# Optimization experiments

Measured on AMD Instinct MI355X. Metric: run time of the kernel, lower is better.

## Reference

```python
import jax, jax.numpy as jnp
import numpy as np

N = 100000      # nodes
E = 1600000     # edges (before self-loops)
FIN = 128       # in_channels
HID = 16        # hidden_channels
H = 8           # heads (layer 1)
OUT = 64        # out_channels
LN_EPS = 1e-5


def setup_inputs() -> dict:
    key = jax.random.key(0)
    ks = jax.random.split(key, 24)
    def p(i, shape):
        return jax.random.normal(ks[i], shape, dtype=jnp.float32) * 0.05
    return {
        "x": jax.random.normal(ks[0], (N, FIN), dtype=jnp.float32),
        "edge_index": jax.random.randint(ks[1], (2, E), 0, N, dtype=jnp.int32),
        # GATv2 layer 1: in -> H*HID, concat
        "Wl1": p(2, (FIN, H * HID)), "bl1": p(3, (H * HID,)),
        "Wr1": p(4, (FIN, H * HID)), "br1": p(5, (H * HID,)),
        "att1": p(6, (H, HID)), "bias1": p(7, (H * HID,)),
        # GATv2 layer 2: H*HID -> HID, heads=1
        "Wl2": p(8, (H * HID, HID)), "bl2": p(9, (HID,)),
        "Wr2": p(10, (H * HID, HID)), "br2": p(11, (HID,)),
        "att2": p(12, (1, HID)), "bias2": p(13, (HID,)),
        # LayerNorms
        "ln1_g": jnp.ones((H * HID,), jnp.float32), "ln1_b": jnp.zeros((H * HID,), jnp.float32),
        "ln2_g": jnp.ones((HID,), jnp.float32), "ln2_b": jnp.zeros((HID,), jnp.float32),
        # residual / skip / output linears
        "res1_W": p(14, (FIN, H * HID)), "res1_b": p(15, (H * HID,)),
        "res2_W": p(16, (H * HID, HID)), "res2_b": p(17, (HID,)),
        "skip_W": p(18, (H * HID, HID)), "skip_b": p(19, (HID,)),
        "out_W": p(20, (HID, OUT)), "out_b": p(21, (OUT,)),
    }


def _layernorm(x, g, b):
    mu = jnp.mean(x, axis=-1, keepdims=True)
    var = jnp.mean((x - mu) ** 2, axis=-1, keepdims=True)
    return (x - mu) * jax.lax.rsqrt(var + LN_EPS) * g + b


def _gatv2(x, src, dst, Wl, bl, Wr, br, att, bias, concat):
    # PyG GATv2Conv (share_weights=False, eval mode): message from src j to dst i
    Hh, C = att.shape
    n = x.shape[0]
    xl = (x @ Wl + bl).reshape(n, Hh, C)   # source-side transform
    xr = (x @ Wr + br).reshape(n, Hh, C)   # target-side transform
    m = xl[src] + xr[dst]                  # [E, H, C]
    e = jax.nn.leaky_relu(m, 0.2)
    alpha = jnp.einsum('ehc,hc->eh', e, att)          # [E, H]
    amax = jax.ops.segment_max(alpha, dst, num_segments=n)
    alpha = jnp.exp(alpha - amax[dst])
    denom = jax.ops.segment_sum(alpha, dst, num_segments=n)
    alpha = alpha / (denom[dst] + 1e-16)
    out = jax.ops.segment_sum(xl[src] * alpha[:, :, None], dst, num_segments=n)  # [N, H, C]
    out = out.reshape(n, Hh * C) if concat else out.mean(axis=1)
    return out + bias


def reference(x, edge_index, Wl1, bl1, Wr1, br1, att1, bias1,
              Wl2, bl2, Wr2, br2, att2, bias2,
              ln1_g, ln1_b, ln2_g, ln2_b,
              res1_W, res1_b, res2_W, res2_b, skip_W, skip_b, out_W, out_b):
    n = x.shape[0]
    loops = jnp.arange(n, dtype=edge_index.dtype)
    src = jnp.concatenate([edge_index[0], loops])
    dst = jnp.concatenate([edge_index[1], loops])

    h = _gatv2(x, src, dst, Wl1, bl1, Wr1, br1, att1, bias1, concat=True)
    h = _layernorm(h, ln1_g, ln1_b)
    h = h + (x @ res1_W + res1_b)
    h = jax.nn.elu(h)            # dropout off in eval

    skip_in = h
    h2 = _gatv2(h, src, dst, Wl2, bl2, Wr2, br2, att2, bias2, concat=False)
    h2 = _layernorm(h2, ln2_g, ln2_b)
    h2 = h2 + (skip_in @ res2_W + res2_b)
    h2 = jax.nn.elu(h2)
    h2 = h2 + (skip_in @ skip_W + skip_b)
    return h2 @ out_W + out_b
```

## Files before the change

### kernel.cpp

```cpp
#include <hip/hip_runtime.h>

typedef __attribute__((ext_vector_type(8))) short bf16x8;
typedef __attribute__((ext_vector_type(4))) float f32x4;

__device__ __forceinline__ float bf2f(ushort u) {
  union { uint i; float f; } v; v.i = ((uint)u) << 16; return v.f;
}
__device__ __forceinline__ ushort f2bf(float f) {
  union { float f; uint i; } v; v.f = f;
  uint r = (v.i + 0x7FFFu + ((v.i >> 16) & 1u)) >> 16;
  return (ushort)r;
}

template <int CTRL>
__device__ __forceinline__ float dppadd(float x) {
  union { float f; int i; } a, b;
  a.f = x;
  b.i = __builtin_amdgcn_update_dpp(0, a.i, CTRL, 0xF, 0xF, true);
  return a.f + b.f;
}
#define DPP_X1 0xB1
#define DPP_X2 0x4E
#define DPP_X7 0x141
#define DPP_XF 0x140


__global__ __launch_bounds__(256) void k_zero(int* p, int n) {
  int i = blockIdx.x * 256 + threadIdx.x;
  if (i < n) p[i] = 0;
}

__global__ __launch_bounds__(256) void k_hist(const int* __restrict__ ei, int* __restrict__ cnt, int E) {
  int e = blockIdx.x * 256 + threadIdx.x;
  if (e < E) atomicAdd(&cnt[ei[E + e]], 1);
}

__global__ __launch_bounds__(256) void k_scan1(const int* __restrict__ cnt, int* __restrict__ partial, int n) {
  int i = blockIdx.x * 256 + threadIdx.x;
  int v = (i < n) ? cnt[i] : 0;
  #pragma unroll
  for (int m = 1; m < 64; m <<= 1) v += __shfl_xor(v, m);
  __shared__ int sm[4];
  if ((threadIdx.x & 63) == 0) sm[threadIdx.x >> 6] = v;
  __syncthreads();
  if (threadIdx.x == 0) partial[blockIdx.x] = sm[0] + sm[1] + sm[2] + sm[3];
}

__global__ __launch_bounds__(512) void k_scan2(int* partial, int nb) {
  __shared__ int buf[2][512];
  int t = threadIdx.x;
  int v = (t < nb) ? partial[t] : 0;
  buf[0][t] = v;
  __syncthreads();
  int cur = 0;
  for (int off = 1; off < 512; off <<= 1) {
    int x = buf[cur][t];
    if (t >= off) x += buf[cur][t - off];
    buf[cur ^ 1][t] = x;
    __syncthreads();
    cur ^= 1;
  }
  if (t < nb) partial[t] = buf[cur][t] - v;
}

__global__ __launch_bounds__(256) void k_scan3(const int* __restrict__ cnt, const int* __restrict__ partial,
                                               int* __restrict__ rowptr, int* __restrict__ cursor, int n) {
  __shared__ int buf[2][256];
  int t = threadIdx.x;
  int i = blockIdx.x * 256 + t;
  int v = (i < n) ? cnt[i] : 0;
  buf[0][t] = v;
  __syncthreads();
  int cur = 0;
  for (int off = 1; off < 256; off <<= 1) {
    int x = buf[cur][t];
    if (t >= off) x += buf[cur][t - off];
    buf[cur ^ 1][t] = x;
    __syncthreads();
    cur ^= 1;
  }
  if (i < n) {
    int incl = buf[cur][t];
    int base = partial[blockIdx.x];
    int rp = base + incl - v;
    rowptr[i] = rp;
    cursor[i] = rp;
    if (i == n - 1) rowptr[n] = base + incl;
  }
}

__global__ __launch_bounds__(256) void k_scatter(const int* __restrict__ ei, int* __restrict__ cursor,
                                                 int* __restrict__ ssrc, int E, int NS) {
  int t = threadIdx.x;
  int base = blockIdx.x * 2048;
  int src[8], dst[8];
  #pragma unroll
  for (int j = 0; j < 8; ++j) {
    int idx = base + j * 256 + t;
    bool ok = idx < E;
    src[j] = ok ? ei[idx] : 0;
    dst[j] = ok ? ei[E + idx] : -1;
  }
  for (int s = 0; s < NS; ++s) {
    #pragma unroll
    for (int j = 0; j < 8; ++j) {
      if ((dst[j] >> 13) == s) {
        int pos = atomicAdd(&cursor[dst[j]], 1);
        ssrc[pos] = src[j];
      }
    }
  }
}


__global__ __launch_bounds__(256) void k_conv(const float* __restrict__ x, ushort* __restrict__ AF, int total) {
  int t = blockIdx.x * 256 + threadIdx.x;
  if (t >= total) return;
  int m = t >> 4, k8 = t & 15;
  const float* src = x + (size_t)m * 128 + k8 * 8;
  float4 f0 = *(const float4*)src;
  float4 f1 = *(const float4*)(src + 4);
  uint4 o;
  o.x = f2bf(f0.x) | ((uint)f2bf(f0.y) << 16);
  o.y = f2bf(f0.z) | ((uint)f2bf(f0.w) << 16);
  o.z = f2bf(f1.x) | ((uint)f2bf(f1.y) << 16);
  o.w = f2bf(f1.z) | ((uint)f2bf(f1.w) << 16);
  size_t off = ((size_t)(((m >> 4) * 4 + (k8 >> 2)) * 64) + (m & 15) + ((k8 & 3) << 4)) * 8;
  *(uint4*)(AF + off) = o;
}


__global__ __launch_bounds__(256) void k_pack(
    const float* __restrict__ Wl1, const float* __restrict__ bl1,
    const float* __restrict__ Wr1, const float* __restrict__ br1,
    const float* __restrict__ res1W, const float* __restrict__ res1b,
    const float* __restrict__ Wl2, const float* __restrict__ bl2,
    const float* __restrict__ Wr2, const float* __restrict__ br2,
    const float* __restrict__ res2W, const float* __restrict__ res2b,
    const float* __restrict__ skipW, const float* __restrict__ skipb,
    const float* __restrict__ att1, const float* __restrict__ att2,
    ushort* __restrict__ W1F, float* __restrict__ B1P,
    ushort* __restrict__ W2F, float* __restrict__ B2P,
    float* __restrict__ attE, float* __restrict__ at2E) {
  const float LOG2E = 1.4426950408889634f;
  int tid = blockIdx.x * 256 + threadIdx.x;
  if (tid < 49152) {
    int j = tid & 7, l = (tid >> 3) & 63, ktile = (tid >> 9) & 3, ct = tid >> 11;
    int k = ktile * 32 + ((l >> 4) << 3) + j;
    int n = ct * 16 + (l & 15);
    int sel = n >> 7, jj = n & 127;
    const float* s = sel == 0 ? Wl1 : sel == 1 ? Wr1 : res1W;
    W1F[tid] = f2bf(s[k * 128 + jj]);
  } else if (tid < 57344) {
    int u = tid - 49152;
    int j = u & 7, l = (u >> 3) & 63, ktile = (u >> 9) & 3, ct = u >> 11;
    int k = ktile * 32 + ((l >> 4) << 3) + j;
    int n = ct * 16 + (l & 15);
    int sel = n >> 4, jj = n & 15;
    const float* s = sel == 0 ? Wl2 : sel == 1 ? Wr2 : sel == 2 ? res2W : skipW;
    W2F[u] = f2bf(s[k * 16 + jj]);
  } else if (tid < 57728) {
    int n = tid - 57344;
    int sel = n >> 7, jj = n & 127;
    const float* sb = sel == 0 ? bl1 : sel == 1 ? br1 : res1b;
    B1P[n] = sb[jj];
  } else if (tid < 57792) {
    int n = tid - 57728;
    int sel = n >> 4, jj = n & 15;
    const float* sb = sel == 0 ? bl2 : sel == 1 ? br2 : sel == 2 ? res2b : skipb;
    B2P[n] = sb[jj];
  } else if (tid < 57920) {
    int n = tid - 57792;
    attE[n] = att1[n] * LOG2E;
  } else if (tid < 57936) {
    int n = tid - 57920;
    at2E[n] = att2[n] * LOG2E;
  }
}


__global__ __launch_bounds__(256) void k_mfma(
    const ushort* __restrict__ AF, const ushort* __restrict__ WF,
    const float* __restrict__ bias,
    ushort* __restrict__ O0, ushort* __restrict__ O1,
    ushort* __restrict__ O2, ushort* __restrict__ O3,
    int M, int cs_shift) {
  int w = threadIdx.x >> 6, l = threadIdx.x & 63;
  int m0 = blockIdx.x * 64;
  int c0 = blockIdx.y * 64 + w * 16;
  int ct = c0 >> 4;
  f32x4 acc[4] = {};
  #pragma unroll
  for (int kt = 0; kt < 4; ++kt) {
    bf16x8 b = *(const bf16x8*)(WF + ((size_t)((ct * 4 + kt) * 64 + l)) * 8);
    #pragma unroll
    for (int rt = 0; rt < 4; ++rt) {
      bf16x8 a = *(const bf16x8*)(AF + ((size_t)((blockIdx.x * 16 + rt * 4 + kt) * 64 + l)) * 8);
      acc[rt] = __builtin_amdgcn_mfma_f32_16x16x32_bf16(a, b, acc[rt], 0, 0, 0);
    }
  }
  int col = c0 + (l & 15);
  int arr = col >> cs_shift;
  ushort* O = arr == 0 ? O0 : arr == 1 ? O1 : arr == 2 ? O2 : O3;
  int stride = 1 << cs_shift;
  int lcol = col & (stride - 1);
  float bv = bias[col];
  int rbase = m0 + ((l >> 4) << 2);
  #pragma unroll
  for (int rt = 0; rt < 4; ++rt) {
    #pragma unroll
    for (int r = 0; r < 4; ++r) {
      int m = rbase + rt * 16 + r;
      if (m < M) O[(size_t)m * stride + lcol] = f2bf(acc[rt][r] + bv);
    }
  }
}


#define EDGE1U(u)                                                          \
  {                                                                        \
    float vx = __builtin_bit_cast(float, (u) << 16);                       \
    float vy = __builtin_bit_cast(float, (u) & 0xffff0000u);               \
    float mx = vx + xr.x, my = vy + xr.y;                                  \
    float ta = atv.x * mx + atv.y * my;                                    \
    float tb = atv.x * __builtin_fabsf(mx) + atv.y * __builtin_fabsf(my);  \
    float tt = 0.6f * ta + 0.4f * tb;                                      \
    tt = dppadd<DPP_X1>(tt);                                               \
    tt = dppadd<DPP_X2>(tt);                                               \
    tt = dppadd<DPP_X7>(tt);                                               \
    float p = __builtin_amdgcn_exp2f(tt);                                  \
    accx += p * vx; accy += p * vy; den += p;                              \
  }

__global__ __launch_bounds__(256) void k_gat1(
    const ushort* __restrict__ XLG, const ushort* __restrict__ XR,
    const ushort* __restrict__ RE,
    const float* __restrict__ attE, const float* __restrict__ bias1,
    const float* __restrict__ g1, const float* __restrict__ b1,
    const int* __restrict__ rowptr, const int* __restrict__ ssrc,
    ushort* __restrict__ HF, int n) {
  int lane = threadIdx.x & 63;
  int i = blockIdx.x * 4 + (threadIdx.x >> 6);
  if (i >= n) return;
  int f = lane * 2;
  size_t ib = (size_t)i << 7;
  uint u_self = *(const uint*)(XLG + ib + f);
  float2 xr;
  { uint u = *(const uint*)(XR + ib + f);
    xr = make_float2(__builtin_bit_cast(float, u << 16),
                     __builtin_bit_cast(float, u & 0xffff0000u)); }
  float2 atv = *(const float2*)&attE[f];
  float accx = 0.f, accy = 0.f, den = 0.f;
  EDGE1U(u_self);
  int e0 = __builtin_amdgcn_readfirstlane(rowptr[i]);
  int e1 = __builtin_amdgcn_readfirstlane(rowptr[i + 1]);
  for (int base = e0; base < e1; base += 64) {
    int cnt = e1 - base; if (cnt > 64) cnt = 64;
    int sidx = ssrc[base + (lane < cnt ? lane : cnt - 1)];
    int j = 0;
    for (; j + 4 <= cnt; j += 4) {
      int s0 = __builtin_amdgcn_readlane(sidx, j);
      int s1 = __builtin_amdgcn_readlane(sidx, j + 1);
      int s2 = __builtin_amdgcn_readlane(sidx, j + 2);
      int s3 = __builtin_amdgcn_readlane(sidx, j + 3);
      uint u0 = *(const uint*)(XLG + ((size_t)(uint)s0 << 7) + f);
      uint u1 = *(const uint*)(XLG + ((size_t)(uint)s1 << 7) + f);
      uint u2 = *(const uint*)(XLG + ((size_t)(uint)s2 << 7) + f);
      uint u3 = *(const uint*)(XLG + ((size_t)(uint)s3 << 7) + f);
      EDGE1U(u0); EDGE1U(u1); EDGE1U(u2); EDGE1U(u3);
    }
    for (; j < cnt; ++j) {
      int s = __builtin_amdgcn_readlane(sidx, j);
      uint u = *(const uint*)(XLG + ((size_t)(uint)s << 7) + f);
      EDGE1U(u);
    }
  }
  float inv = 1.f / (den + 1e-16f);
  float2 bv = *(const float2*)&bias1[f];
  float ox = accx * inv + bv.x, oy = accy * inv + bv.y;
  float s = ox + oy;
  #pragma unroll
  for (int m = 1; m < 64; m <<= 1) s += __shfl_xor(s, m);
  float mu = s * (1.f / 128.f);
  float dx = ox - mu, dy = oy - mu;
  float q = dx * dx + dy * dy;
  #pragma unroll
  for (int m = 1; m < 64; m <<= 1) q += __shfl_xor(q, m);
  float rstd = rsqrtf(q * (1.f / 128.f) + 1e-5f);
  float2 gg = *(const float2*)&g1[f];
  float2 bb = *(const float2*)&b1[f];
  float2 rv;
  { uint u = *(const uint*)(RE + ib + f);
    rv = make_float2(__builtin_bit_cast(float, u << 16),
                     __builtin_bit_cast(float, u & 0xffff0000u)); }
  float yx = dx * rstd * gg.x + bb.x + rv.x;
  float yy = dy * rstd * gg.y + bb.y + rv.y;
  yx = yx > 0.f ? yx : __expf(yx) - 1.f;
  yy = yy > 0.f ? yy : __expf(yy) - 1.f;
  size_t off = (((size_t)(i >> 4) * 4 + (lane >> 4)) * 64 + (i & 15) + ((lane >> 2) & 3) * 16) * 8
               + 2 * (lane & 3);
  *(uint*)(HF + off) = (uint)f2bf(yx) | ((uint)f2bf(yy) << 16);
}


#define EDGE2V(v)                                            \
  {                                                          \
    float m = (v) + xr;                                      \
    float ta = a2 * m;                                       \
    float tb = a2 * __builtin_fabsf(m);                      \
    float tt = 0.6f * ta + 0.4f * tb;                        \
    tt = dppadd<DPP_X1>(tt);                                 \
    tt = dppadd<DPP_X2>(tt);                                 \
    tt = dppadd<DPP_X7>(tt);                                 \
    tt = dppadd<DPP_XF>(tt);                                 \
    float p = __builtin_amdgcn_exp2f(tt);                    \
    acc += p * (v); den += p;                                \
  }

__global__ __launch_bounds__(256) void k_gat2(
    const ushort* __restrict__ XG, const ushort* __restrict__ XRr,
    const ushort* __restrict__ XE, const ushort* __restrict__ XS,
    const float* __restrict__ at2E, const float* __restrict__ bias2,
    const float* __restrict__ g2, const float* __restrict__ b2,
    const int* __restrict__ rowptr, const int* __restrict__ ssrc,
    const float* __restrict__ outW, const float* __restrict__ outB,
    float* __restrict__ Out, int n) {
  __shared__ float sW[1024];
  __shared__ float sB[64];
  int t = threadIdx.x;
  for (int idx = t; idx < 1024; idx += 256) sW[idx] = outW[idx];
  if (t < 64) sB[t] = outB[t];
  __syncthreads();
  int c = t & 15;
  int i = blockIdx.x * 16 + (t >> 4);
  if (i >= n) return;
  size_t ib = (size_t)i << 4;
  float xl = bf2f(XG[ib + c]), xr = bf2f(XRr[ib + c]);
  float resv = bf2f(XE[ib + c]), skipv = bf2f(XS[ib + c]);
  float a2 = at2E[c];
  float acc = 0.f, den = 0.f;
  EDGE2V(xl);
  int e0 = rowptr[i], e1 = rowptr[i + 1];
  int e = e0;
  for (; e + 4 <= e1; e += 4) {
    int s0 = ssrc[e], s1 = ssrc[e + 1], s2 = ssrc[e + 2], s3 = ssrc[e + 3];
    float v0 = bf2f(XG[((size_t)(uint)s0 << 4) + c]);
    float v1 = bf2f(XG[((size_t)(uint)s1 << 4) + c]);
    float v2 = bf2f(XG[((size_t)(uint)s2 << 4) + c]);
    float v3 = bf2f(XG[((size_t)(uint)s3 << 4) + c]);
    EDGE2V(v0); EDGE2V(v1); EDGE2V(v2); EDGE2V(v3);
  }
  for (; e < e1; ++e) {
    int s = ssrc[e];
    float v = bf2f(XG[((size_t)(uint)s << 4) + c]);
    EDGE2V(v);
  }
  float o = acc / (den + 1e-16f) + bias2[c];
  float s = o;
  s = dppadd<DPP_X1>(s); s = dppadd<DPP_X2>(s); s = dppadd<DPP_X7>(s); s = dppadd<DPP_XF>(s);
  float mu = s * (1.f / 16.f);
  float d = o - mu;
  float q = d * d;
  q = dppadd<DPP_X1>(q); q = dppadd<DPP_X2>(q); q = dppadd<DPP_X7>(q); q = dppadd<DPP_XF>(q);
  float rstd = rsqrtf(q * (1.f / 16.f) + 1e-5f);
  float y = d * rstd * g2[c] + b2[c] + resv;
  y = y > 0.f ? y : __expf(y) - 1.f;
  y += skipv;
  float a0 = sB[c * 4 + 0], a1 = sB[c * 4 + 1], ao2 = sB[c * 4 + 2], a3 = sB[c * 4 + 3];
  #pragma unroll
  for (int cc = 0; cc < 16; ++cc) {
    float h = __shfl(y, cc, 16);
    a0 += h * sW[cc * 64 + c * 4 + 0];
    a1 += h * sW[cc * 64 + c * 4 + 1];
    ao2 += h * sW[cc * 64 + c * 4 + 2];
    a3 += h * sW[cc * 64 + c * 4 + 3];
  }
  *(float4*)&Out[(size_t)i * 64 + c * 4] = make_float4(a0, a1, ao2, a3);
}


extern "C" void kernel_launch(void* const* d_in, const int* in_sizes, int n_in,
                              void* d_out, int out_size, void* d_ws, size_t ws_size,
                              hipStream_t stream) {
  const float* x     = (const float*)d_in[0];
  const int*   ei    = (const int*)d_in[1];
  const float* Wl1   = (const float*)d_in[2];
  const float* bl1   = (const float*)d_in[3];
  const float* Wr1   = (const float*)d_in[4];
  const float* br1   = (const float*)d_in[5];
  const float* att1  = (const float*)d_in[6];
  const float* bias1 = (const float*)d_in[7];
  const float* Wl2   = (const float*)d_in[8];
  const float* bl2   = (const float*)d_in[9];
  const float* Wr2   = (const float*)d_in[10];
  const float* br2   = (const float*)d_in[11];
  const float* att2  = (const float*)d_in[12];
  const float* bias2 = (const float*)d_in[13];
  const float* ln1g  = (const float*)d_in[14];
  const float* ln1b  = (const float*)d_in[15];
  const float* ln2g  = (const float*)d_in[16];
  const float* ln2b  = (const float*)d_in[17];
  const float* res1W = (const float*)d_in[18];
  const float* res1b = (const float*)d_in[19];
  const float* res2W = (const float*)d_in[20];
  const float* res2b = (const float*)d_in[21];
  const float* skipW = (const float*)d_in[22];
  const float* skipb = (const float*)d_in[23];
  const float* outW  = (const float*)d_in[24];
  const float* outb  = (const float*)d_in[25];
  int N = in_sizes[0] / 128;
  int E = in_sizes[1] / 2;
  float* out = (float*)d_out;

  int nblk = (N + 63) / 64;
  int ngrp = nblk * 4;

  ushort* XF   = (ushort*)d_ws;
  ushort* XLG  = XF + (size_t)ngrp * 2048;
  ushort* XR1  = XLG + (size_t)N * 128;
  ushort* RE1  = XR1 + (size_t)N * 128;
  ushort* HF   = RE1 + (size_t)N * 128;
  ushort* XG2  = HF + (size_t)ngrp * 2048;
  ushort* X2R  = XG2 + (size_t)N * 16;
  ushort* X2E  = X2R + (size_t)N * 16;
  ushort* X2S  = X2E + (size_t)N * 16;
  ushort* W1F  = X2S + (size_t)N * 16;
  ushort* W2F  = W1F + 49152;
  float*  B1P  = (float*)(W2F + 8192);
  float*  B2P  = B1P + 384;
  float*  attE = B2P + 64;
  float*  at2E = attE + 128;
  int* cnt     = (int*)(at2E + 16);
  int* cursor  = cnt + N;
  int* rowptr  = cursor + N;
  int* ssrc    = rowptr + N + 1;
  int* partial = ssrc + E;

  int nbS = (N + 255) / 256;
  int nbE = (E + 255) / 256;
  int NS = ((N - 1) >> 13) + 1;

  k_pack<<<227, 256, 0, stream>>>(Wl1, bl1, Wr1, br1, res1W, res1b,
                                  Wl2, bl2, Wr2, br2, res2W, res2b, skipW, skipb,
                                  att1, att2, W1F, B1P, W2F, B2P, attE, at2E);
  k_conv<<<(N * 16 + 255) / 256, 256, 0, stream>>>(x, XF, N * 16);

  k_zero<<<nbS, 256, 0, stream>>>(cnt, N);
  k_hist<<<nbE, 256, 0, stream>>>(ei, cnt, E);
  k_scan1<<<nbS, 256, 0, stream>>>(cnt, partial, N);
  k_scan2<<<1, 512, 0, stream>>>(partial, nbS);
  k_scan3<<<nbS, 256, 0, stream>>>(cnt, partial, rowptr, cursor, N);
  k_scatter<<<(E + 2047) / 2048, 256, 0, stream>>>(ei, cursor, ssrc, E, NS);

  dim3 g1g(nblk, 6);
  k_mfma<<<g1g, 256, 0, stream>>>(XF, W1F, B1P, XLG, XR1, RE1, XLG, N, 7);

  k_gat1<<<(N + 3) / 4, 256, 0, stream>>>(XLG, XR1, RE1, attE, bias1, ln1g, ln1b,
                                          rowptr, ssrc, HF, N);

  dim3 g2g(nblk, 1);
  k_mfma<<<g2g, 256, 0, stream>>>(HF, W2F, B2P, XG2, X2R, X2E, X2S, N, 4);
  k_gat2<<<(N + 15) / 16, 256, 0, stream>>>(XG2, X2R, X2E, X2S, at2E, bias2, ln2g, ln2b,
                                            rowptr, ssrc, outW, outb, out, N);
}
```

Measured before the change: 487.6 us.

## Fuse setup kernels, merge scatter with GEMM, and widen gat1 edge loads

Merges weight packing, x conversion and count zeroing into one init kernel. The scan2 pass is dropped because each scan3 block now sums its preceding partials itself. CSR scatter and the layer-1 MFMA GEMM run as independent blocks of one launch, and the histogram processes four edges per thread. The gat1 kernel is restructured so each half-wave handles a different edge with 4 features per lane, using pre-split 0.6/0.4 attention weights to simplify the leaky-relu dot product. Together these aim to cut launch count and the per-edge reduction cost, at the price of more complex indexing and redundant partial summation in the scan.

```diff
diff --git a/kernel.cpp b/kernel.cpp
--- a/kernel.cpp
+++ b/kernel.cpp
@@ -11,6 +11,8 @@
   uint r = (v.i + 0x7FFFu + ((v.i >> 16) & 1u)) >> 16;
   return (ushort)r;
 }
+__device__ __forceinline__ float blo(uint u) { return __builtin_bit_cast(float, u << 16); }
+__device__ __forceinline__ float bhi(uint u) { return __builtin_bit_cast(float, u & 0xffff0000u); }
 
 template <int CTRL>
 __device__ __forceinline__ float dppadd(float x) {
@@ -25,15 +27,93 @@
 #define DPP_XF 0x140
 
 
-__global__ __launch_bounds__(256) void k_zero(int* p, int n) {
-  int i = blockIdx.x * 256 + threadIdx.x;
-  if (i < n) p[i] = 0;
-}
+__global__ __launch_bounds__(256) void k_init(
+    const float* __restrict__ x, ushort* __restrict__ XF,
+    const float* __restrict__ Wl1, const float* __restrict__ bl1,
+    const float* __restrict__ Wr1, const float* __restrict__ br1,
+    const float* __restrict__ res1W, const float* __restrict__ res1b,
+    const float* __restrict__ Wl2, const float* __restrict__ bl2,
+    const float* __restrict__ Wr2, const float* __restrict__ br2,
+    const float* __restrict__ res2W, const float* __restrict__ res2b,
+    const float* __restrict__ skipW, const float* __restrict__ skipb,
+    const float* __restrict__ att1, const float* __restrict__ att2,
+    ushort* __restrict__ W1F, float* __restrict__ B1P,
+    ushort* __restrict__ W2F, float* __restrict__ B2P,
+    float* __restrict__ at6, float* __restrict__ at4, float* __restrict__ at2E,
+    int* __restrict__ cnt, int N) {
+  const float LOG2E = 1.4426950408889634f;
+  int b = blockIdx.x, t = threadIdx.x;
+  int CB = (N * 16 + 255) >> 8;
+  if (b < 227) {
+    int tid = b * 256 + t;
+    if (tid < 49152) {
+      int j = tid & 7, l = (tid >> 3) & 63, ktile = (tid >> 9) & 3, ct = tid >> 11;
+      int k = ktile * 32 + ((l >> 4) << 3) + j;
+      int n = ct * 16 + (l & 15);
+      int sel = n >> 7, jj = n & 127;
+      const float* s = sel == 0 ? Wl1 : sel == 1 ? Wr1 : res1W;
+      W1F[tid] = f2bf(s[k * 128 + jj]);
+    } else if (tid < 57344) {
+      int u = tid - 49152;
+      int j = u & 7, l = (u >> 3) & 63, ktile = (u >> 9) & 3, ct = u >> 11;
+      int k = ktile * 32 + ((l >> 4) << 3) + j;
+      int n = ct * 16 + (l & 15);
+      int sel = n >> 4, jj = n & 15;
+      const float* s = sel == 0 ? Wl2 : sel == 1 ? Wr2 : sel == 2 ? res2W : skipW;
+      W2F[u] = f2bf(s[k * 16 + jj]);
+    } else if (tid < 57728) {
+      int n = tid - 57344;
+      int sel = n >> 7, jj = n & 127;
+      const float* sb = sel == 0 ? bl1 : sel == 1 ? br1 : res1b;
+      B1P[n] = sb[jj];
+    } else if (tid < 57792) {
+      int n = tid - 57728;
+      int sel = n >> 4, jj = n & 15;
+      const float* sb = sel == 0 ? bl2 : sel == 1 ? br2 : sel == 2 ? res2b : skipb;
+      B2P[n] = sb[jj];
+    } else if (tid < 57920) {
+      int n = tid - 57792;
+      at6[n] = att1[n] * 0.6f * LOG2E;
+    } else if (tid < 58048) {
+      int n = tid - 57920;
+      at4[n] = att1[n] * 0.4f * LOG2E;
+    } else if (tid < 58064) {
+      int n = tid - 58048;
+      at2E[n] = att2[n] * LOG2E;
+    }
+  } else if (b < 227 + CB) {
+    int t2 = (b - 227) * 256 + t;
+    if (t2 < N * 16) {
+      int m = t2 >> 4, k8 = t2 & 15;
+      const float* src = x + (size_t)m * 128 + k8 * 8;
+      float4 f0 = *(const float4*)src;
+      float4 f1 = *(const float4*)(src + 4);
+      uint4 o;
+      o.x = f2bf(f0.x) | ((uint)f2bf(f0.y) << 16);
+      o.y = f2bf(f0.z) | ((uint)f2bf(f0.w) << 16);
+      o.z = f2bf(f1.x) | ((uint)f2bf(f1.y) << 16);
+      o.w = f2bf(f1.z) | ((uint)f2bf(f1.w) << 16);
+      size_t off = ((size_t)(((m >> 4) * 4 + (k8 >> 2)) * 64) + (m & 15) + ((k8 & 3) << 4)) * 8;
+      *(uint4*)(XF + off) = o;
+    }
+  } else {
+    int idx = (b - 227 - CB) * 256 + t;
+    if (idx < N) cnt[idx] = 0;
+  }
+}
+
 
 __global__ __launch_bounds__(256) void k_hist(const int* __restrict__ ei, int* __restrict__ cnt, int E) {
-  int e = blockIdx.x * 256 + threadIdx.x;
-  if (e < E) atomicAdd(&cnt[ei[E + e]], 1);
-}
+  int e4 = (blockIdx.x * 256 + threadIdx.x) * 4;
+  if (e4 + 3 < E) {
+    int4 d = *(const int4*)&ei[E + e4];
+    atomicAdd(&cnt[d.x], 1); atomicAdd(&cnt[d.y], 1);
+    atomicAdd(&cnt[d.z], 1); atomicAdd(&cnt[d.w], 1);
+  } else {
+    for (int e = e4; e < E; ++e) atomicAdd(&cnt[ei[E + e]], 1);
+  }
+}
+
 
 __global__ __launch_bounds__(256) void k_scan1(const int* __restrict__ cnt, int* __restrict__ partial, int n) {
   int i = blockIdx.x * 256 + threadIdx.x;
@@ -46,28 +126,21 @@
   if (threadIdx.x == 0) partial[blockIdx.x] = sm[0] + sm[1] + sm[2] + sm[3];
 }
 
-__global__ __launch_bounds__(512) void k_scan2(int* partial, int nb) {
-  __shared__ int buf[2][512];
+
+__global__ __launch_bounds__(256) void k_scan3lb(const int* __restrict__ cnt, const int* __restrict__ partial,
+                                                 int* __restrict__ rowptr, int* __restrict__ cursor, int n) {
   int t = threadIdx.x;
-  int v = (t < nb) ? partial[t] : 0;
-  buf[0][t] = v;
+  int b = blockIdx.x;
+  int acc = 0;
+  for (int j = t; j < b; j += 256) acc += partial[j];
+  #pragma unroll
+  for (int m = 1; m < 64; m <<= 1) acc += __shfl_xor(acc, m);
+  __shared__ int sm[4];
+  if ((t & 63) == 0) sm[t >> 6] = acc;
   __syncthreads();
-  int cur = 0;
-  for (int off = 1; off < 512; off <<= 1) {
-    int x = buf[cur][t];
-    if (t >= off) x += buf[cur][t - off];
-    buf[cur ^ 1][t] = x;
-    __syncthreads();
-    cur ^= 1;
-  }
-  if (t < nb) partial[t] = buf[cur][t] - v;
-}
-
-__global__ __launch_bounds__(256) void k_scan3(const int* __restrict__ cnt, const int* __restrict__ partial,
-                                               int* __restrict__ rowptr, int* __restrict__ cursor, int n) {
+  int base = sm[0] + sm[1] + sm[2] + sm[3];
   __shared__ int buf[2][256];
-  int t = threadIdx.x;
-  int i = blockIdx.x * 256 + t;
+  int i = b * 256 + t;
   int v = (i < n) ? cnt[i] : 0;
   buf[0][t] = v;
   __syncthreads();
@@ -81,7 +154,6 @@
   }
   if (i < n) {
     int incl = buf[cur][t];
-    int base = partial[blockIdx.x];
     int rp = base + incl - v;
     rowptr[i] = rp;
     cursor[i] = rp;
@@ -89,105 +161,77 @@
   }
 }
 
-__global__ __launch_bounds__(256) void k_scatter(const int* __restrict__ ei, int* __restrict__ cursor,
-                                                 int* __restrict__ ssrc, int E, int NS) {
+
+__global__ __launch_bounds__(256) void k_scatgemm(
+    const int* __restrict__ ei, int* __restrict__ cursor, int* __restrict__ ssrc, int E, int NS, int nScat,
+    const ushort* __restrict__ AF, const ushort* __restrict__ WF, const float* __restrict__ bias,
+    ushort* __restrict__ O0, ushort* __restrict__ O1, ushort* __restrict__ O2,
+    int M, int nblk) {
+  int b = blockIdx.x;
   int t = threadIdx.x;
-  int base = blockIdx.x * 2048;
-  int src[8], dst[8];
-  #pragma unroll
-  for (int j = 0; j < 8; ++j) {
-    int idx = base + j * 256 + t;
-    bool ok = idx < E;
-    src[j] = ok ? ei[idx] : 0;
-    dst[j] = ok ? ei[E + idx] : -1;
-  }
-  for (int s = 0; s < NS; ++s) {
+  if (b < nScat) {
+    int base = b * 2048;
+    int src[8], dst[8];
     #pragma unroll
     for (int j = 0; j < 8; ++j) {
-      if ((dst[j] >> 13) == s) {
-        int pos = atomicAdd(&cursor[dst[j]], 1);
-        ssrc[pos] = src[j];
+      int idx = base + j * 256 + t;
+      bool ok = idx < E;
+      src[j] = ok ? ei[idx] : 0;
+      dst[j] = ok ? ei[E + idx] : -1;
+    }
+    for (int s = 0; s < NS; ++s) {
+      #pragma unroll
+      for (int j = 0; j < 8; ++j) {
+        if ((dst[j] >> 13) == s) {
+          int pos = atomicAdd(&cursor[dst[j]], 1);
+          ssrc[pos] = src[j];
+        }
       }
     }
-  }
-}
-
-
-__global__ __launch_bounds__(256) void k_conv(const float* __restrict__ x, ushort* __restrict__ AF, int total) {
-  int t = blockIdx.x * 256 + threadIdx.x;
-  if (t >= total) return;
-  int m = t >> 4, k8 = t & 15;
-  const float* src = x + (size_t)m * 128 + k8 * 8;
-  float4 f0 = *(const float4*)src;
-  float4 f1 = *(const float4*)(src + 4);
-  uint4 o;
-  o.x = f2bf(f0.x) | ((uint)f2bf(f0.y) << 16);
-  o.y = f2bf(f0.z) | ((uint)f2bf(f0.w) << 16);
-  o.z = f2bf(f1.x) | ((uint)f2bf(f1.y) << 16);
-  o.w = f2bf(f1.z) | ((uint)f2bf(f1.w) << 16);
-  size_t off = ((size_t)(((m >> 4) * 4 + (k8 >> 2)) * 64) + (m & 15) + ((k8 & 3) << 4)) * 8;
-  *(uint4*)(AF + off) = o;
-}
-
-
-__global__ __launch_bounds__(256) void k_pack(
-    const float* __restrict__ Wl1, const float* __restrict__ bl1,
-    const float* __restrict__ Wr1, const float* __restrict__ br1,
-    const float* __restrict__ res1W, const float* __restrict__ res1b,
-    const float* __restrict__ Wl2, const float* __restrict__ bl2,
-    const float* __restrict__ Wr2, const float* __restrict__ br2,
-    const float* __restrict__ res2W, const float* __restrict__ res2b,
-    const float* __restrict__ skipW, const float* __restrict__ skipb,
-    const float* __restrict__ att1, const float* __restrict__ att2,
-    ushort* __restrict__ W1F, float* __restrict__ B1P,
-    ushort* __restrict__ W2F, float* __restrict__ B2P,
-    float* __restrict__ attE, float* __restrict__ at2E) {
-  const float LOG2E = 1.4426950408889634f;
-  int tid = blockIdx.x * 256 + threadIdx.x;
-  if (tid < 49152) {
-    int j = tid & 7, l = (tid >> 3) & 63, ktile = (tid >> 9) & 3, ct = tid >> 11;
-    int k = ktile * 32 + ((l >> 4) << 3) + j;
-    int n = ct * 16 + (l & 15);
-    int sel = n >> 7, jj = n & 127;
-    const float* s = sel == 0 ? Wl1 : sel == 1 ? Wr1 : res1W;
-    W1F[tid] = f2bf(s[k * 128 + jj]);
-  } else if (tid < 57344) {
-    int u = tid - 49152;
-    int j = u & 7, l = (u >> 3) & 63, ktile = (u >> 9) & 3, ct = u >> 11;
-    int k = ktile * 32 + ((l >> 4) << 3) + j;
-    int n = ct * 16 + (l & 15);
-    int sel = n >> 4, jj = n & 15;
-    const float* s = sel == 0 ? Wl2 : sel == 1 ? Wr2 : sel == 2 ? res2W : skipW;
-    W2F[u] = f2bf(s[k * 16 + jj]);
-  } else if (tid < 57728) {
-    int n = tid - 57344;
-    int sel = n >> 7, jj = n & 127;
-    const float* sb = sel == 0 ? bl1 : sel == 1 ? br1 : res1b;
-    B1P[n] = sb[jj];
-  } else if (tid < 57792) {
-    int n = tid - 57728;
-    int sel = n >> 4, jj = n & 15;
-    const float* sb = sel == 0 ? bl2 : sel == 1 ? br2 : sel == 2 ? res2b : skipb;
-    B2P[n] = sb[jj];
-  } else if (tid < 57920) {
-    int n = tid - 57792;
-    attE[n] = att1[n] * LOG2E;
-  } else if (tid < 57936) {
-    int n = tid - 57920;
-    at2E[n] = att2[n] * LOG2E;
-  }
-}
-
-
-__global__ __launch_bounds__(256) void k_mfma(
+  } else {
+    int bb = b - nScat;
+    int by = bb / nblk;
+    int bx = bb - by * nblk;
+    int w = t >> 6, l = t & 63;
+    int m0 = bx * 64;
+    int c0 = by * 64 + w * 16;
+    int ct = c0 >> 4;
+    f32x4 acc[4] = {};
+    #pragma unroll
+    for (int kt = 0; kt < 4; ++kt) {
+      bf16x8 bfr = *(const bf16x8*)(WF + ((size_t)((ct * 4 + kt) * 64 + l)) * 8);
+      #pragma unroll
+      for (int rt = 0; rt < 4; ++rt) {
+        bf16x8 a = *(const bf16x8*)(AF + ((size_t)((bx * 16 + rt * 4 + kt) * 64 + l)) * 8);
+        acc[rt] = __builtin_amdgcn_mfma_f32_16x16x32_bf16(a, bfr, acc[rt], 0, 0, 0);
+      }
+    }
+    int col = c0 + (l & 15);
+    int arr = col >> 7;
+    ushort* O = arr == 0 ? O0 : arr == 1 ? O1 : O2;
+    int lcol = col & 127;
+    float bv = bias[col];
+    int rbase = m0 + ((l >> 4) << 2);
+    #pragma unroll
+    for (int rt = 0; rt < 4; ++rt) {
+      #pragma unroll
+      for (int r = 0; r < 4; ++r) {
+        int m = rbase + rt * 16 + r;
+        if (m < M) O[(size_t)m * 128 + lcol] = f2bf(acc[rt][r] + bv);
+      }
+    }
+  }
+}
+
+
+__global__ __launch_bounds__(256) void k_mfma2(
     const ushort* __restrict__ AF, const ushort* __restrict__ WF,
     const float* __restrict__ bias,
     ushort* __restrict__ O0, ushort* __restrict__ O1,
-    ushort* __restrict__ O2, ushort* __restrict__ O3,
-    int M, int cs_shift) {
+    ushort* __restrict__ O2, ushort* __restrict__ O3, int M) {
   int w = threadIdx.x >> 6, l = threadIdx.x & 63;
   int m0 = blockIdx.x * 64;
-  int c0 = blockIdx.y * 64 + w * 16;
+  int c0 = w * 16;
   int ct = c0 >> 4;
   f32x4 acc[4] = {};
   #pragma unroll
@@ -200,10 +244,9 @@
     }
   }
   int col = c0 + (l & 15);
-  int arr = col >> cs_shift;
+  int arr = col >> 4;
   ushort* O = arr == 0 ? O0 : arr == 1 ? O1 : arr == 2 ? O2 : O3;
-  int stride = 1 << cs_shift;
-  int lcol = col & (stride - 1);
+  int lcol = col & 15;
   float bv = bias[col];
   int rbase = m0 + ((l >> 4) << 2);
   #pragma unroll
@@ -211,47 +254,53 @@
     #pragma unroll
     for (int r = 0; r < 4; ++r) {
       int m = rbase + rt * 16 + r;
-      if (m < M) O[(size_t)m * stride + lcol] = f2bf(acc[rt][r] + bv);
-    }
-  }
-}
-
-
-#define EDGE1U(u)                                                          \
-  {                                                                        \
-    float vx = __builtin_bit_cast(float, (u) << 16);                       \
-    float vy = __builtin_bit_cast(float, (u) & 0xffff0000u);               \
-    float mx = vx + xr.x, my = vy + xr.y;                                  \
-    float ta = atv.x * mx + atv.y * my;                                    \
-    float tb = atv.x * __builtin_fabsf(mx) + atv.y * __builtin_fabsf(my);  \
-    float tt = 0.6f * ta + 0.4f * tb;                                      \
-    tt = dppadd<DPP_X1>(tt);                                               \
-    tt = dppadd<DPP_X2>(tt);                                               \
-    tt = dppadd<DPP_X7>(tt);                                               \
-    float p = __builtin_amdgcn_exp2f(tt);                                  \
-    accx += p * vx; accy += p * vy; den += p;                              \
+      if (m < M) O[(size_t)m * 16 + lcol] = f2bf(acc[rt][r] + bv);
+    }
+  }
+}
+
+
+#define EDGE1B(u, MASKHI)                                              \
+  {                                                                    \
+    float v0 = blo((u).x), v1 = bhi((u).x);                            \
+    float v2 = blo((u).y), v3 = bhi((u).y);                            \
+    float m0 = v0 + xr0, m1 = v1 + xr1, m2 = v2 + xr2, m3 = v3 + xr3;  \
+    float d = a6.x * m0 + a4.x * __builtin_fabsf(m0);                  \
+    d += a6.y * m1; d += a4.y * __builtin_fabsf(m1);                   \
+    d += a6.z * m2; d += a4.z * __builtin_fabsf(m2);                   \
+    d += a6.w * m3; d += a4.w * __builtin_fabsf(m3);                   \
+    d = dppadd<DPP_X1>(d);                                             \
+    d = dppadd<DPP_X2>(d);                                             \
+    float p = __builtin_amdgcn_exp2f(d);                               \
+    if (MASKHI) p = hi ? 0.f : p;                                      \
+    acc0 += p * v0; acc1 += p * v1; acc2 += p * v2; acc3 += p * v3;    \
+    den += p;                                                          \
   }
 
 __global__ __launch_bounds__(256) void k_gat1(
     const ushort* __restrict__ XLG, const ushort* __restrict__ XR,
     const ushort* __restrict__ RE,
-    const float* __restrict__ attE, const float* __restrict__ bias1,
+    const float* __restrict__ at6, const float* __restrict__ at4,
+    const float* __restrict__ bias1,
     const float* __restrict__ g1, const float* __restrict__ b1,
     const int* __restrict__ rowptr, const int* __restrict__ ssrc,
     ushort* __restrict__ HF, int n) {
   int lane = threadIdx.x & 63;
   int i = blockIdx.x * 4 + (threadIdx.x >> 6);
   if (i >= n) return;
-  int f = lane * 2;
-  size_t ib = (size_t)i << 7;
-  uint u_self = *(const uint*)(XLG + ib + f);
-  float2 xr;
-  { uint u = *(const uint*)(XR + ib + f);
-    xr = make_float2(__builtin_bit_cast(float, u << 16),
-                     __builtin_bit_cast(float, u & 0xffff0000u)); }
-  float2 atv = *(const float2*)&attE[f];
-  float accx = 0.f, accy = 0.f, den = 0.f;
-  EDGE1U(u_self);
+  int l32 = lane & 31;
+  bool hi = lane >= 32;
+  int fb = l32 * 4;
+  size_t rowb = (size_t)i << 8;
+  uint2 uxr = *(const uint2*)((const char*)XR + rowb + (fb << 1));
+  float xr0 = blo(uxr.x), xr1 = bhi(uxr.x), xr2 = blo(uxr.y), xr3 = bhi(uxr.y);
+  float4 a6 = *(const float4*)&at6[fb];
+  float4 a4 = *(const float4*)&at4[fb];
+  float acc0 = 0.f, acc1 = 0.f, acc2 = 0.f, acc3 = 0.f, den = 0.f;
+  {
+    uint2 us = *(const uint2*)((const char*)XLG + rowb + (fb << 1));
+    EDGE1B(us, true);
+  }
   int e0 = __builtin_amdgcn_readfirstlane(rowptr[i]);
   int e1 = __builtin_amdgcn_readfirstlane(rowptr[i + 1]);
   for (int base = e0; base < e1; base += 64) {
@@ -263,43 +312,64 @@
       int s1 = __builtin_amdgcn_readlane(sidx, j + 1);
       int s2 = __builtin_amdgcn_readlane(sidx, j + 2);
       int s3 = __builtin_amdgcn_readlane(sidx, j + 3);
-      uint u0 = *(const uint*)(XLG + ((size_t)(uint)s0 << 7) + f);
-      uint u1 = *(const uint*)(XLG + ((size_t)(uint)s1 << 7) + f);
-      uint u2 = *(const uint*)(XLG + ((size_t)(uint)s2 << 7) + f);
-      uint u3 = *(const uint*)(XLG + ((size_t)(uint)s3 << 7) + f);
-      EDGE1U(u0); EDGE1U(u1); EDGE1U(u2); EDGE1U(u3);
-    }
-    for (; j < cnt; ++j) {
-      int s = __builtin_amdgcn_readlane(sidx, j);
-      uint u = *(const uint*)(XLG + ((size_t)(uint)s << 7) + f);
-      EDGE1U(u);
-    }
-  }
+      int rA = hi ? s1 : s0;
+      int rB = hi ? s3 : s2;
+      uint2 uA = *(const uint2*)((const char*)XLG + ((size_t)(uint)rA << 8) + (fb << 1));
+      uint2 uB = *(const uint2*)((const char*)XLG + ((size_t)(uint)rB << 8) + (fb << 1));
+      EDGE1B(uA, false);
+      EDGE1B(uB, false);
+    }
+    for (; j + 2 <= cnt; j += 2) {
+      int s0 = __builtin_amdgcn_readlane(sidx, j);
+      int s1 = __builtin_amdgcn_readlane(sidx, j + 1);
+      int r = hi ? s1 : s0;
+      uint2 u = *(const uint2*)((const char*)XLG + ((size_t)(uint)r << 8) + (fb << 1));
+      EDGE1B(u, false);
+    }
+    if (j < cnt) {
+      int s0 = __builtin_amdgcn_readlane(sidx, j);
+      uint2 u = *(const uint2*)((const char*)XLG + ((size_t)(uint)s0 << 8) + (fb << 1));
+      EDGE1B(u, true);
+    }
+  }
+  acc0 += __shfl_xor(acc0, 32);
+  acc1 += __shfl_xor(acc1, 32);
+  acc2 += __shfl_xor(acc2, 32);
+  acc3 += __shfl_xor(acc3, 32);
+  den  += __shfl_xor(den, 32);
   float inv = 1.f / (den + 1e-16f);
-  float2 bv = *(const float2*)&bias1[f];
-  float ox = accx * inv + bv.x, oy = accy * inv + bv.y;
-  float s = ox + oy;
-  #pragma unroll
-  for (int m = 1; m < 64; m <<= 1) s += __shfl_xor(s, m);
+  float4 bv = *(const float4*)&bias1[fb];
+  float o0 = acc0 * inv + bv.x, o1 = acc1 * inv + bv.y;
+  float o2 = acc2 * inv + bv.z, o3 = acc3 * inv + bv.w;
+  float s = o0 + o1 + o2 + o3;
+  #pragma unroll
+  for (int m = 1; m < 32; m <<= 1) s += __shfl_xor(s, m);
   float mu = s * (1.f / 128.f);
-  float dx = ox - mu, dy = oy - mu;
-  float q = dx * dx + dy * dy;
-  #pragma unroll
-  for (int m = 1; m < 64; m <<= 1) q += __shfl_xor(q, m);
+  float d0 = o0 - mu, d1 = o1 - mu, d2 = o2 - mu, d3 = o3 - mu;
+  float q = d0 * d0 + d1 * d1 + d2 * d2 + d3 * d3;
+  #pragma unroll
+  for (int m = 1; m < 32; m <<= 1) q += __shfl_xor(q, m);
   float rstd = rsqrtf(q * (1.f / 128.f) + 1e-5f);
-  float2 gg = *(const float2*)&g1[f];
-  float2 bb = *(const float2*)&b1[f];
-  float2 rv;
-  { uint u = *(const uint*)(RE + ib + f);
-    rv = make_float2(__builtin_bit_cast(float, u << 16),
-                     __builtin_bit_cast(float, u & 0xffff0000u)); }
-  float yx = dx * rstd * gg.x + bb.x + rv.x;
-  float yy = dy * rstd * gg.y + bb.y + rv.y;
-  yx = yx > 0.f ? yx : __expf(yx) - 1.f;
-  yy = yy > 0.f ? yy : __expf(yy) - 1.f;
-  size_t off = (((size_t)(i >> 4) * 4 + (lane >> 4)) * 64 + (i & 15) + ((lane >> 2) & 3) * 16) * 8
-               + 2 * (lane & 3);
-  *(uint*)(HF + off) = (uint)f2bf(yx) | ((uint)f2bf(yy) << 16);
+  float4 gg = *(const float4*)&g1[fb];
+  float4 bb = *(const float4*)&b1[fb];
+  uint2 ur = *(const uint2*)((const char*)RE + rowb + (fb << 1));
+  float r0 = blo(ur.x), r1 = bhi(ur.x), r2 = blo(ur.y), r3 = bhi(ur.y);
+  float y0 = d0 * rstd * gg.x + bb.x + r0;
+  float y1 = d1 * rstd * gg.y + bb.y + r1;
+  float y2 = d2 * rstd * gg.z + bb.z + r2;
+  float y3 = d3 * rstd * gg.w + bb.w + r3;
+  y0 = y0 > 0.f ? y0 : __expf(y0) - 1.f;
+  y1 = y1 > 0.f ? y1 : __expf(y1) - 1.f;
+  y2 = y2 > 0.f ? y2 : __expf(y2) - 1.f;
+  y3 = y3 > 0.f ? y3 : __expf(y3) - 1.f;
+  if (!hi) {
+    int k8 = l32 >> 1;
+    size_t slot = ((size_t)(i >> 4) * 4 + (k8 >> 2)) * 64 + (i & 15) + ((k8 & 3) << 4);
+    uint2 o;
+    o.x = (uint)f2bf(y0) | ((uint)f2bf(y1) << 16);
+    o.y = (uint)f2bf(y2) | ((uint)f2bf(y3) << 16);
+    *(uint2*)(HF + slot * 8 + (l32 & 1) * 4) = o;
+  }
 }
 
 
@@ -428,8 +498,9 @@
   ushort* W2F  = W1F + 49152;
   float*  B1P  = (float*)(W2F + 8192);
   float*  B2P  = B1P + 384;
-  float*  attE = B2P + 64;
-  float*  at2E = attE + 128;
+  float*  at6  = B2P + 64;
+  float*  at4  = at6 + 128;
+  float*  at2E = at4 + 128;
   int* cnt     = (int*)(at2E + 16);
   int* cursor  = cnt + N;
   int* rowptr  = cursor + N;
@@ -437,29 +508,22 @@
   int* partial = ssrc + E;
 
   int nbS = (N + 255) / 256;
-  int nbE = (E + 255) / 256;
-  int NS = ((N - 1) >> 13) + 1;
-
-  k_pack<<<227, 256, 0, stream>>>(Wl1, bl1, Wr1, br1, res1W, res1b,
-                                  Wl2, bl2, Wr2, br2, res2W, res2b, skipW, skipb,
-                                  att1, att2, W1F, B1P, W2F, B2P, attE, at2E);
-  k_conv<<<(N * 16 + 255) / 256, 256, 0, stream>>>(x, XF, N * 16);
-
-  k_zero<<<nbS, 256, 0, stream>>>(cnt, N);
-  k_hist<<<nbE, 256, 0, stream>>>(ei, cnt, E);
+  int CB  = (N * 16 + 255) / 256;
+  int NS  = ((N - 1) >> 13) + 1;
+  int nScat = (E + 2047) / 2048;
+
+  k_init<<<227 + CB + nbS, 256, 0, stream>>>(x, XF, Wl1, bl1, Wr1, br1, res1W, res1b,
+                                             Wl2, bl2, Wr2, br2, res2W, res2b, skipW, skipb,
+                                             att1, att2, W1F, B1P, W2F, B2P, at6, at4, at2E,
+                                             cnt, N);
+  k_hist<<<(E + 1023) / 1024, 256, 0, stream>>>(ei, cnt, E);
   k_scan1<<<nbS, 256, 0, stream>>>(cnt, partial, N);
-  k_scan2<<<1, 512, 0, stream>>>(partial, nbS);
-  k_scan3<<<nbS, 256, 0, stream>>>(cnt, partial, rowptr, cursor, N);
-  k_scatter<<<(E + 2047) / 2048, 256, 0, stream>>>(ei, cursor, ssrc, E, NS);
-
-  dim3 g1g(nblk, 6);
-  k_mfma<<<g1g, 256, 0, stream>>>(XF, W1F, B1P, XLG, XR1, RE1, XLG, N, 7);
-
-  k_gat1<<<(N + 3) / 4, 256, 0, stream>>>(XLG, XR1, RE1, attE, bias1, ln1g, ln1b,
+  k_scan3lb<<<nbS, 256, 0, stream>>>(cnt, partial, rowptr, cursor, N);
+  k_scatgemm<<<nScat + nblk * 6, 256, 0, stream>>>(ei, cursor, ssrc, E, NS, nScat,
+                                                   XF, W1F, B1P, XLG, XR1, RE1, N, nblk);
+  k_gat1<<<(N + 3) / 4, 256, 0, stream>>>(XLG, XR1, RE1, at6, at4, bias1, ln1g, ln1b,
                                           rowptr, ssrc, HF, N);
-
-  dim3 g2g(nblk, 1);
-  k_mfma<<<g2g, 256, 0, stream>>>(HF, W2F, B2P, XG2, X2R, X2E, X2S, N, 4);
+  k_mfma2<<<nblk, 256, 0, stream>>>(HF, W2F, B2P, XG2, X2R, X2E, X2S, N);
   k_gat2<<<(N + 15) / 16, 256, 0, stream>>>(XG2, X2R, X2E, X2S, at2E, bias2, ln2g, ln2b,
                                             rowptr, ssrc, outW, outb, out, N);
 }
```

Measured after the change: 459.0 us. 1.06x faster.
